# Kernel optimization log

Hardware: AMD Instinct MI355X
Metric: run time of the kernel (lower is better)

Reference implementation:

```python
import jax, jax.numpy as jnp
import numpy as np

N, E, F, H, D = 4096, 65536, 128, 128, 3
RATIO = 0.5
SLOPE = 0.01  # LeakyReLU negative slope (torch default)


def setup_inputs() -> dict:
    key = jax.random.key(0)
    ks = jax.random.split(key, 8)
    s = 1.0 / np.sqrt(H)
    x = jax.random.normal(ks[0], (N, F), dtype=jnp.float32)
    edge_index = jax.random.randint(ks[1], (2, E), 0, N, dtype=jnp.int64)
    Wd = jax.random.normal(ks[2], (D + 1, F, H), dtype=jnp.float32) * s
    bd = jax.random.normal(ks[3], (D + 1, H), dtype=jnp.float32) * 0.01
    Wu = jax.random.normal(ks[4], (D, H, H), dtype=jnp.float32) * s
    bu = jax.random.normal(ks[5], (D, H), dtype=jnp.float32) * 0.01
    pw = jax.random.normal(ks[6], (D, H), dtype=jnp.float32) * s
    return dict(x=x, edge_index=edge_index, Wd=Wd, bd=bd, Wu=Wu, bu=bu, pw=pw)


def gcn(x, A, W, b):
    # GCNConv(improved=True): self-loop fill value 2; A[i, j] = weight of edge j -> i
    A2 = A + 2.0 * jnp.eye(A.shape[0], dtype=A.dtype)
    deg = A2.sum(axis=1)
    dinv = jnp.where(deg > 0, jax.lax.rsqrt(deg), 0.0)
    Ahat = dinv[:, None] * A2 * dinv[None, :]
    return Ahat @ (x @ W) + b


def augment(A):
    # GraphUNet.augment_adj: remove self loops, add self loops (w=1), A @ A (spspmm), remove self loops
    n = A.shape[0]
    eye = jnp.eye(n, dtype=A.dtype)
    A1 = A * (1.0 - eye) + eye
    B = A1 @ A1
    return B * (1.0 - eye)


def topk_pool(x, A, w, k):
    # TopKPooling: score = tanh(x @ w / ||w||); keep top-k nodes (descending)
    score = jnp.tanh((x @ w) / jnp.linalg.norm(w))
    top, perm = jax.lax.top_k(score, k)
    xp = x[perm] * top[:, None]
    Ap = A[perm][:, perm]
    return xp, Ap, perm


def reference(x, edge_index, Wd, bd, Wu, bu, pw):
    act = lambda v: jax.nn.leaky_relu(v, SLOPE)
    # dense adjacency in [dst, src] convention; duplicate edges sum (coalesce)
    A = jnp.zeros((N, N), jnp.float32).at[edge_index[1], edge_index[0]].add(1.0)
    x = act(gcn(x, A, Wd[0], bd[0]))
    xs, As, perms = [x], [A], []
    n = N
    for i in range(1, D + 1):
        A = augment(A)
        k = int(np.ceil(RATIO * n))
        n = k
        x, A, perm = topk_pool(x, A, pw[i - 1], k)
        x = act(gcn(x, A, Wd[i], bd[i]))
        if i < D:
            xs.append(x)
            As.append(A)
        perms.append(perm)
    for i in range(D):
        j = D - 1 - i
        res, Aj, perm = xs[j], As[j], perms[j]
        up = jnp.zeros_like(res).at[perm].set(x)  # unpool: scatter into kept slots
        x = res + up  # sum_res=True
        x = gcn(x, Aj, Wu[i], bu[i])
        if i < D - 1:
            x = act(x)
    return x  # [N, out_dim]
```

## Files before the change

kernel.cpp:

```cpp
#include <hip/hip_runtime.h>

typedef unsigned short u16;
typedef __attribute__((ext_vector_type(4))) short s16x4;
typedef __attribute__((ext_vector_type(8))) short s16x8;
typedef __attribute__((ext_vector_type(4))) float f32x4;

__device__ __forceinline__ float bf2f_(u16 b) { return __uint_as_float(((unsigned)b) << 16); }
__device__ __forceinline__ u16 f2bf_(float f) {
  unsigned u = __float_as_uint(f);
  return (u16)((u + 0x7FFFu + ((u >> 16) & 1u)) >> 16);
}

__device__ __forceinline__ void edge_decode(const int* ei, int e, int E, const int* flags,
                                            int& src, int& dst) {
  bool is64 = flags[1] < 100;
  src = is64 ? ei[2 * e] : ei[e];
  dst = is64 ? ei[2 * E + 2 * e] : ei[E + e];
}

__global__ void k_zeroi(int* a, int n) {
  int i = blockIdx.x * 256 + threadIdx.x;
  if (i < n) a[i] = 0;
}

__global__ __launch_bounds__(256) void k_detect(const u16* __restrict__ xb,
                                                const int* __restrict__ ei,
                                                int* __restrict__ flags) {
  int i = blockIdx.x * 256 + threadIdx.x;
  int e8 = (xb[2 * i] >> 7) & 0xFF;
  int sane = (e8 >= 100 && e8 <= 140) ? 1 : 0;
  int nz = (ei[2 * i + 1] != 0) ? 1 : 0;
  #pragma unroll
  for (int off = 32; off; off >>= 1) { sane += __shfl_down(sane, off); nz += __shfl_down(nz, off); }
  if ((threadIdx.x & 63) == 0) { atomicAdd(&flags[0], sane); atomicAdd(&flags[1], nz); }
}

__global__ void k_loadall(const void* x, const void* wd, const void* bd, const void* wu,
                          const void* bu, const void* pw,
                          float* xin, float* Wdf, float* bdf, float* Wuf, float* buf_, float* pwf,
                          const int* __restrict__ flags) {
  int i = blockIdx.x * 256 + threadIdx.x;
  const void* src; float* dst; int off;
  if (i < 524288) { src = x; dst = xin; off = i; }
  else if (i < 589824) { src = wd; dst = Wdf; off = i - 524288; }
  else if (i < 590336) { src = bd; dst = bdf; off = i - 589824; }
  else if (i < 639488) { src = wu; dst = Wuf; off = i - 590336; }
  else if (i < 639872) { src = bu; dst = buf_; off = i - 639488; }
  else if (i < 640256) { src = pw; dst = pwf; off = i - 639872; }
  else return;
  bool isbf = flags[0] >= 2048;
  dst[off] = isbf ? bf2f_(((const u16*)src)[off]) : ((const float*)src)[off];
}

__global__ void k_fill0(float4* __restrict__ p, long n4) {
  long i = blockIdx.x * 256L + threadIdx.x;
  long stride = (long)gridDim.x * 256L;
  for (; i < n4; i += stride) p[i] = make_float4(0.f, 0.f, 0.f, 0.f);
}

__global__ void k_diag0(float* __restrict__ C, int M) {
  int i = blockIdx.x * 256 + threadIdx.x;
  if (i < M) C[(size_t)i * M + i] = 0.f;
}

__global__ void k_degcnt(const int* __restrict__ ei, int E, int n, const int* __restrict__ flags,
                         int* __restrict__ indeg, int* __restrict__ outdeg, int* __restrict__ indeg2) {
  int e = blockIdx.x * 256 + threadIdx.x;
  if (e >= E) return;
  int src, dst; edge_decode(ei, e, E, flags, src, dst);
  if (src < 0 || src >= n || dst < 0 || dst >= n) return;
  atomicAdd(&indeg2[dst], 1);
  if (src == dst) return;
  atomicAdd(&indeg[dst], 1);
  atomicAdd(&outdeg[src], 1);
}

__global__ __launch_bounds__(1024) void k_scan3(const int* __restrict__ d0, const int* __restrict__ d1,
                                                const int* __restrict__ d2,
                                                int* o0, int* o1, int* o2,
                                                int* c0, int* c1, int* c2, int n) {
  __shared__ int part[1024];
  int t = threadIdx.x;
  int per = n / 1024;
  for (int pass = 0; pass < 3; ++pass) {
    const int* deg = pass == 0 ? d0 : (pass == 1 ? d1 : d2);
    int* off = pass == 0 ? o0 : (pass == 1 ? o1 : o2);
    int* cur = pass == 0 ? c0 : (pass == 1 ? c1 : c2);
    int local[8];
    int s = 0;
    for (int j = 0; j < per; ++j) { local[j] = s; s += deg[t * per + j]; }
    part[t] = s;
    __syncthreads();
    for (int d = 1; d < 1024; d <<= 1) {
      int v = (t >= d) ? part[t - d] : 0;
      __syncthreads();
      part[t] += v;
      __syncthreads();
    }
    int base = (t == 0) ? 0 : part[t - 1];
    for (int j = 0; j < per; ++j) {
      off[t * per + j] = base + local[j];
      cur[t * per + j] = base + local[j];
    }
    if (t == 1023) off[n] = part[1023];
    __syncthreads();
  }
}

__global__ void k_csrfill(const int* __restrict__ ei, int E, int n, const int* __restrict__ flags,
                          int* __restrict__ incur, int* __restrict__ outcur, int* __restrict__ incur2,
                          int* __restrict__ inlist, int* __restrict__ outlist, int* __restrict__ inlist2) {
  int e = blockIdx.x * 256 + threadIdx.x;
  if (e >= E) return;
  int src, dst; edge_decode(ei, e, E, flags, src, dst);
  if (src < 0 || src >= n || dst < 0 || dst >= n) return;
  inlist2[atomicAdd(&incur2[dst], 1)] = src;
  if (src == dst) return;
  inlist[atomicAdd(&incur[dst], 1)] = src;
  outlist[atomicAdd(&outcur[src], 1)] = dst;
}

__global__ __launch_bounds__(256) void k_rowsort(const int* __restrict__ inoff2,
                                                 const int* __restrict__ inlist2,
                                                 int* __restrict__ outlist2, int n) {
  int wave = threadIdx.x >> 6, lane = threadIdx.x & 63;
  int row = blockIdx.x * 4 + wave;
  if (row >= n) return;
  int ib = inoff2[row], ie = inoff2[row + 1];
  int L = ie - ib;
  for (int i = lane; i < L; i += 64) {
    int ki = inlist2[ib + i];
    int rank = 0;
    for (int j = 0; j < L; ++j) {
      int kj = inlist2[ib + j];
      rank += (kj < ki || (kj == ki && j < i)) ? 1 : 0;
    }
    outlist2[ib + rank] = ki;
  }
}

__global__ void k_dinvcsr(const int* __restrict__ indeg2, float* __restrict__ dinv, int n) {
  int i = blockIdx.x * 256 + threadIdx.x;
  if (i < n) dinv[i] = rsqrtf((float)indeg2[i] + 2.0f);
}

__global__ __launch_bounds__(256) void k_spool(const int* __restrict__ inoff, const int* __restrict__ inlist,
                                               const int* __restrict__ outoff, const int* __restrict__ outlist,
                                               const int* __restrict__ inv, float* __restrict__ C,
                                               int M, int n) {
  int wave = threadIdx.x >> 6, lane = threadIdx.x & 63;
  int v = blockIdx.x * 4 + wave;
  if (v >= n) return;
  int ib = inoff[v], ni = inoff[v + 1] - ib;
  int ob = outoff[v], no = outoff[v + 1] - ob;
  int tot = ni * no;
  for (int p = lane; p < tot; p += 64) {
    int oi = p / ni, ii = p - oi * ni;
    int i = outlist[ob + oi];
    int j = inlist[ib + ii];
    if (i == j) continue;
    int ri = inv[i], rj = inv[j];
    if (ri >= 0 && rj >= 0) atomicAdd(&C[(size_t)ri * M + rj], 1.0f);
  }
}

__global__ void k_spedge(const int* __restrict__ ei, int E, int n, const int* __restrict__ flags,
                         const int* __restrict__ inv, float* __restrict__ C, int M) {
  int e = blockIdx.x * 256 + threadIdx.x;
  if (e >= E) return;
  int src, dst; edge_decode(ei, e, E, flags, src, dst);
  if (src < 0 || src >= n || dst < 0 || dst >= n || src == dst) return;
  int ri = inv[dst], rj = inv[src];
  if (ri >= 0 && rj >= 0) atomicAdd(&C[(size_t)ri * M + rj], 2.0f);
}

__global__ __launch_bounds__(256) void k_dinv(const float* __restrict__ A, float* __restrict__ dinv, int n) {
  int row = blockIdx.x;
  const float* r = A + (size_t)row * n;
  float s = 0.f;
  for (int j = threadIdx.x; j < n; j += 256) s += r[j];
  #pragma unroll
  for (int off = 32; off; off >>= 1) s += __shfl_down(s, off);
  __shared__ float red[4];
  int wave = threadIdx.x >> 6, lane = threadIdx.x & 63;
  if (lane == 0) red[wave] = s;
  __syncthreads();
  if (threadIdx.x == 0) {
    float deg = red[0] + red[1] + red[2] + red[3] + 2.0f;
    dinv[row] = rsqrtf(deg);
  }
}

__global__ __launch_bounds__(256) void k_xw(const float* __restrict__ x, const float* __restrict__ W,
                                            const float* __restrict__ dinv, float* __restrict__ yp, int n) {
  __shared__ float xs_[16 * 128];
  int t = threadIdx.x;
  int row0 = blockIdx.x * 16;
  for (int e = t; e < 16 * 128; e += 256) {
    int r = e >> 7, c = e & 127;
    xs_[e] = x[(size_t)(row0 + r) * 128 + c];
  }
  __syncthreads();
  int c = t & 127, rh = t >> 7;
  float acc[8];
  #pragma unroll
  for (int ri = 0; ri < 8; ++ri) acc[ri] = 0.f;
  for (int k = 0; k < 128; ++k) {
    float wv = W[k * 128 + c];
    #pragma unroll
    for (int ri = 0; ri < 8; ++ri) acc[ri] += xs_[(rh * 8 + ri) * 128 + k] * wv;
  }
  #pragma unroll
  for (int ri = 0; ri < 8; ++ri) {
    int r = row0 + rh * 8 + ri;
    yp[(size_t)r * 128 + c] = dinv[r] * acc[ri];
  }
}

template<int FINAL>
__global__ __launch_bounds__(256) void k_spmv(const int* __restrict__ inoff2, const int* __restrict__ inlist2,
                                              const float* __restrict__ y, const float* __restrict__ dinv,
                                              const float* __restrict__ b,
                                              float* __restrict__ outf, void* __restrict__ outv,
                                              int n, int act, const int* __restrict__ flags) {
  int wave = threadIdx.x >> 6, lane = threadIdx.x & 63;
  int i = blockIdx.x * 4 + wave;
  if (i >= n) return;
  int ib = inoff2[i], ie = inoff2[i + 1];
  float z0 = 0.f, z1 = 0.f;
  for (int e = ib; e < ie; ++e) {
    int s = inlist2[e];
    z0 += y[(size_t)s * 128 + lane];
    z1 += y[(size_t)s * 128 + 64 + lane];
  }
  float di = dinv[i];
  float y0 = y[(size_t)i * 128 + lane], y1 = y[(size_t)i * 128 + 64 + lane];
  float v0 = di * (z0 + 2.0f * y0) + b[lane];
  float v1 = di * (z1 + 2.0f * y1) + b[64 + lane];
  if (act) { v0 = (v0 >= 0.f) ? v0 : 0.01f * v0; v1 = (v1 >= 0.f) ? v1 : 0.01f * v1; }
  if (FINAL) {
    if (flags[0] >= 2048) {
      ((u16*)outv)[(size_t)i * 128 + lane] = f2bf_(v0);
      ((u16*)outv)[(size_t)i * 128 + 64 + lane] = f2bf_(v1);
    } else {
      ((float*)outv)[(size_t)i * 128 + lane] = v0;
      ((float*)outv)[(size_t)i * 128 + 64 + lane] = v1;
    }
  } else {
    outf[(size_t)i * 128 + lane] = v0;
    outf[(size_t)i * 128 + 64 + lane] = v1;
  }
}

__global__ __launch_bounds__(256) void k_ytr(const float* __restrict__ y,
                                             u16* __restrict__ yTh, u16* __restrict__ yTl, int n) {
  __shared__ float tile[32][129];
  int t = threadIdx.x;
  int r0 = blockIdx.x * 32;
  #pragma unroll
  for (int it = 0; it < 4; ++it) {
    int q = it * 256 + t;
    int r = q >> 5, c4 = (q & 31) * 4;
    float4 v = *(const float4*)&y[(size_t)(r0 + r) * 128 + c4];
    tile[r][c4] = v.x; tile[r][c4 + 1] = v.y; tile[r][c4 + 2] = v.z; tile[r][c4 + 3] = v.w;
  }
  __syncthreads();
  #pragma unroll
  for (int it = 0; it < 2; ++it) {
    int q = it * 256 + t;
    int c = q >> 2, r8 = (q & 3) * 8;
    s16x8 h, l;
    #pragma unroll
    for (int j = 0; j < 8; ++j) {
      float v = tile[r8 + j][c];
      u16 hb = f2bf_(v);
      h[j] = (short)hb;
      l[j] = (short)f2bf_(v - bf2f_(hb));
    }
    *(s16x8*)&yTh[(size_t)c * n + r0 + r8] = h;
    *(s16x8*)&yTl[(size_t)c * n + r0 + r8] = l;
  }
}

template<int ALO>
__global__ __launch_bounds__(256) void k_zgemm_mfma(const float* __restrict__ A,
                                                    const u16* __restrict__ yTh,
                                                    const u16* __restrict__ yTl,
                                                    float* __restrict__ zpart,
                                                    int n, int kchunk) {
  __shared__ __align__(16) u16 ah_[128 * 64];
  __shared__ __align__(16) u16 al_[ALO ? 128 * 64 : 8];
  __shared__ __align__(16) u16 bh_[128 * 64];
  __shared__ __align__(16) u16 bl_[128 * 64];
  int t = threadIdx.x;
  int row0 = blockIdx.x * 128;
  int s = blockIdx.y;
  int kbase = s * kchunk;
  int wave = t >> 6, lane = t & 63;
  int wr = wave >> 1, wc = wave & 1;
  int lrow = lane & 15, kb = lane >> 4;
  const f32x4 z4 = {0.f, 0.f, 0.f, 0.f};
  f32x4 acc[4][4];
  #pragma unroll
  for (int a = 0; a < 4; ++a)
    #pragma unroll
    for (int b = 0; b < 4; ++b) acc[a][b] = z4;

  for (int k0 = 0; k0 < kchunk; k0 += 64) {
    int koff = kbase + k0;
    __syncthreads();
    #pragma unroll
    for (int it = 0; it < 8; ++it) {
      int q = it * 256 + t;
      int r = q >> 4, i4 = q & 15;
      int g = i4 >> 1, h4 = (i4 & 1) * 4;
      float4 v = *(const float4*)&A[(size_t)(row0 + r) * n + koff + i4 * 4];
      float vv[4] = {v.x, v.y, v.z, v.w};
      s16x4 hh, ll;
      #pragma unroll
      for (int j = 0; j < 4; ++j) {
        u16 hb = f2bf_(vv[j]);
        hh[j] = (short)hb;
        if (ALO) ll[j] = (short)f2bf_(vv[j] - bf2f_(hb));
      }
      int ld = r * 64 + ((g ^ (r & 7)) << 3) + h4;
      *(s16x4*)&ah_[ld] = hh;
      if (ALO) *(s16x4*)&al_[ld] = ll;
    }
    #pragma unroll
    for (int it = 0; it < 4; ++it) {
      int q = it * 256 + t;
      int r = q >> 3, g = q & 7;
      int ld = r * 64 + ((g ^ (r & 7)) << 3);
      *(s16x8*)&bh_[ld] = *(const s16x8*)(yTh + (size_t)r * n + koff + g * 8);
      *(s16x8*)&bl_[ld] = *(const s16x8*)(yTl + (size_t)r * n + koff + g * 8);
    }
    __syncthreads();
    #pragma unroll
    for (int ks = 0; ks < 2; ++ks) {
      int gg = ks * 4 + kb;
      int gsw = (gg ^ (lrow & 7)) << 3;
      s16x8 af[4], alf[4], bhf[4], blf[4];
      #pragma unroll
      for (int mi = 0; mi < 4; ++mi) {
        int row = wr * 64 + mi * 16 + lrow;
        af[mi] = *(const s16x8*)&ah_[row * 64 + gsw];
        if (ALO) alf[mi] = *(const s16x8*)&al_[row * 64 + gsw];
      }
      #pragma unroll
      for (int ni = 0; ni < 4; ++ni) {
        int row = wc * 64 + ni * 16 + lrow;
        bhf[ni] = *(const s16x8*)&bh_[row * 64 + gsw];
        blf[ni] = *(const s16x8*)&bl_[row * 64 + gsw];
      }
      #pragma unroll
      for (int mi = 0; mi < 4; ++mi)
        #pragma unroll
        for (int ni = 0; ni < 4; ++ni) {
          acc[mi][ni] = __builtin_amdgcn_mfma_f32_16x16x32_bf16(af[mi], bhf[ni], acc[mi][ni], 0, 0, 0);
          acc[mi][ni] = __builtin_amdgcn_mfma_f32_16x16x32_bf16(af[mi], blf[ni], acc[mi][ni], 0, 0, 0);
          if (ALO) {
            acc[mi][ni] = __builtin_amdgcn_mfma_f32_16x16x32_bf16(alf[mi], bhf[ni], acc[mi][ni], 0, 0, 0);
            acc[mi][ni] = __builtin_amdgcn_mfma_f32_16x16x32_bf16(alf[mi], blf[ni], acc[mi][ni], 0, 0, 0);
          }
        }
    }
  }
  int rbase = (lane >> 4) * 4;
  #pragma unroll
  for (int mi = 0; mi < 4; ++mi)
    #pragma unroll
    for (int ni = 0; ni < 4; ++ni)
      #pragma unroll
      for (int j = 0; j < 4; ++j) {
        int gi = row0 + wr * 64 + mi * 16 + rbase + j;
        int gj = wc * 64 + ni * 16 + (lane & 15);
        zpart[((size_t)s * n + gi) * 128 + gj] = acc[mi][ni][j];
      }
}

__global__ void k_epi(const float* __restrict__ zpart, const float* __restrict__ yp,
                      const float* __restrict__ dinv, const float* __restrict__ b,
                      float* __restrict__ outf, int tot, int act, int n, int S) {
  int i = blockIdx.x * 256 + threadIdx.x;
  if (i >= tot) return;
  int r = i >> 7, c = i & 127;
  float z = 0.f;
  for (int s = 0; s < S; ++s) z += zpart[((size_t)s * n + r) * 128 + c];
  float v = dinv[r] * (z + 2.0f * yp[i]) + b[c];
  if (act) v = (v >= 0.f) ? v : 0.01f * v;
  outf[i] = v;
}

__global__ __launch_bounds__(256) void k_score(const float* __restrict__ x, const float* __restrict__ w,
                                               float* __restrict__ ts, int n) {
  int wave = threadIdx.x >> 6, lane = threadIdx.x & 63;
  int row = blockIdx.x * 4 + wave;
  float w0 = w[lane], w1 = w[64 + lane];
  float nrm = w0 * w0 + w1 * w1;
  #pragma unroll
  for (int off = 32; off; off >>= 1) nrm += __shfl_down(nrm, off);
  nrm = sqrtf(__shfl(nrm, 0));
  if (row < n) {
    const float* xr = x + (size_t)row * 128;
    float d = xr[lane] * w0 + xr[64 + lane] * w1;
    #pragma unroll
    for (int off = 32; off; off >>= 1) d += __shfl_down(d, off);
    if (lane == 0) ts[row] = tanhf(d / nrm);
  }
}

__global__ __launch_bounds__(256) void k_rank(const float* __restrict__ ts, int n, int k,
                                              int* __restrict__ perm, int* __restrict__ inv) {
  int wave = threadIdx.x >> 6, lane = threadIdx.x & 63;
  int i = blockIdx.x * 4 + wave;
  if (i >= n) return;
  unsigned bits = __float_as_uint(ts[i]);
  unsigned u = (bits & 0x80000000u) ? ~bits : (bits | 0x80000000u);
  unsigned long long my = ((unsigned long long)u << 32) | (unsigned)(0xFFFFFFFFu - (unsigned)i);
  int rank = 0;
  for (int j = lane; j < n; j += 64) {
    unsigned b2 = __float_as_uint(ts[j]);
    unsigned u2 = (b2 & 0x80000000u) ? ~b2 : (b2 | 0x80000000u);
    unsigned long long kj = ((unsigned long long)u2 << 32) | (unsigned)(0xFFFFFFFFu - (unsigned)j);
    rank += (kj > my) ? 1 : 0;
  }
  #pragma unroll
  for (int off = 32; off; off >>= 1) rank += __shfl_down(rank, off);
  if (lane == 0) {
    if (rank < k) perm[rank] = i;
    inv[i] = (rank < k) ? rank : -1;
  }
}

__global__ void k_gather(const float* __restrict__ x, const int* __restrict__ perm,
                         const float* __restrict__ ts, float* __restrict__ out, int k) {
  int i = blockIdx.x * 256 + threadIdx.x;
  if (i < k * 128) {
    int r = i >> 7, c = i & 127;
    int p = perm[r];
    out[i] = x[(size_t)p * 128 + c] * ts[p];
  }
}

__global__ void k_unpool(const float* __restrict__ res, const float* __restrict__ prev,
                         const int* __restrict__ inv, float* __restrict__ dst, int tot) {
  int idx = blockIdx.x * 256 + threadIdx.x;
  if (idx >= tot) return;
  int r = idx >> 7, c = idx & 127;
  int ir = inv[r];
  float v = res[idx];
  if (ir >= 0) v += prev[(size_t)ir * 128 + c];
  dst[idx] = v;
}

__global__ __launch_bounds__(256) void k_prep(const float* __restrict__ A, u16* __restrict__ A1,
                                              u16* __restrict__ A1T, int n) {
  __shared__ float tile[32][33];
  int bi = blockIdx.y, bj = blockIdx.x;
  int tx = threadIdx.x & 31, ty = threadIdx.x >> 5;
  int r0 = bi * 32, c0 = bj * 32;
  #pragma unroll
  for (int yy = 0; yy < 4; ++yy) {
    int r = ty * 4 + yy;
    int gr = r0 + r, gc = c0 + tx;
    float v = A[(size_t)gr * n + gc];
    if (gr == gc) v = 1.0f;
    tile[r][tx] = v;
    A1[(size_t)gr * n + gc] = f2bf_(v);
  }
  __syncthreads();
  #pragma unroll
  for (int yy = 0; yy < 4; ++yy) {
    int r = ty * 4 + yy;
    int gr = c0 + r, gc = r0 + tx;
    A1T[(size_t)gr * n + gc] = f2bf_(tile[tx][r]);
  }
}

__global__ __launch_bounds__(256) void k_mfma_pool(const u16* __restrict__ A1, const u16* __restrict__ A1T,
                                                   const int* __restrict__ perm, float* __restrict__ C,
                                                   int M, int K, int kchunk) {
  __shared__ __align__(16) u16 a_lds[128 * 64];
  __shared__ __align__(16) u16 b_lds[128 * 64];
  __shared__ int pr[128], pc[128];
  int t = threadIdx.x;
  int br = blockIdx.x, bc = blockIdx.y;
  int kbase = blockIdx.z * kchunk;
  if (t < 128) pr[t] = perm[br * 128 + t];
  else pc[t - 128] = perm[bc * 128 + (t - 128)];
  __syncthreads();
  int wave = t >> 6, lane = t & 63;
  int wr = wave >> 1, wc = wave & 1;
  int lrow = lane & 15, kb = lane >> 4;
  const f32x4 z4 = {0.f, 0.f, 0.f, 0.f};
  f32x4 acc[4][4];
  #pragma unroll
  for (int a = 0; a < 4; ++a)
    #pragma unroll
    for (int b = 0; b < 4; ++b) acc[a][b] = z4;

  for (int k0 = 0; k0 < kchunk; k0 += 64) {
    int koff = kbase + k0;
    __syncthreads();
    #pragma unroll
    for (int it = 0; it < 4; ++it) {
      int q = it * 256 + t;
      int r = q >> 3, g = q & 7;
      int ld = r * 64 + ((g ^ (r & 7)) << 3);
      *(s16x8*)&a_lds[ld] = *(const s16x8*)(A1 + (size_t)pr[r] * K + koff + g * 8);
      *(s16x8*)&b_lds[ld] = *(const s16x8*)(A1T + (size_t)pc[r] * K + koff + g * 8);
    }
    __syncthreads();
    #pragma unroll
    for (int ks = 0; ks < 2; ++ks) {
      int gg = ks * 4 + kb;
      int gsw = (gg ^ (lrow & 7)) << 3;
      s16x8 af[4], bfv[4];
      #pragma unroll
      for (int mi = 0; mi < 4; ++mi)
        af[mi] = *(const s16x8*)&a_lds[(wr * 64 + mi * 16 + lrow) * 64 + gsw];
      #pragma unroll
      for (int ni = 0; ni < 4; ++ni)
        bfv[ni] = *(const s16x8*)&b_lds[(wc * 64 + ni * 16 + lrow) * 64 + gsw];
      #pragma unroll
      for (int mi = 0; mi < 4; ++mi)
        #pragma unroll
        for (int ni = 0; ni < 4; ++ni)
          acc[mi][ni] = __builtin_amdgcn_mfma_f32_16x16x32_bf16(af[mi], bfv[ni], acc[mi][ni], 0, 0, 0);
    }
  }
  int rbase = (lane >> 4) * 4;
  #pragma unroll
  for (int mi = 0; mi < 4; ++mi)
    #pragma unroll
    for (int ni = 0; ni < 4; ++ni)
      #pragma unroll
      for (int j = 0; j < 4; ++j) {
        int gi = br * 128 + wr * 64 + mi * 16 + rbase + j;
        int gj = bc * 128 + wc * 64 + ni * 16 + (lane & 15);
        atomicAdd(&C[(size_t)gi * M + gj], acc[mi][ni][j]);
      }
}

static void run_gcn_dense(hipStream_t s, const float* A, int n, const float* xinp,
                          const float* W, const float* b, float* dinv, int compute_dinv, float* tmpY,
                          u16* yTh, u16* yTl, float* zpart, int alo, int act, float* outf) {
  if (compute_dinv) k_dinv<<<n, 256, 0, s>>>(A, dinv, n);
  k_xw<<<n / 16, 256, 0, s>>>(xinp, W, dinv, tmpY, n);
  k_ytr<<<n / 32, 256, 0, s>>>(tmpY, yTh, yTl, n);
  int S = (n >= 2048) ? 16 : (n == 1024 ? 8 : 4);
  int kchunk = n / S;
  if (alo)
    k_zgemm_mfma<1><<<dim3(n / 128, S), 256, 0, s>>>(A, yTh, yTl, zpart, n, kchunk);
  else
    k_zgemm_mfma<0><<<dim3(n / 128, S), 256, 0, s>>>(A, yTh, yTl, zpart, n, kchunk);
  int tot = n * 128;
  k_epi<<<(tot + 255) / 256, 256, 0, s>>>(zpart, tmpY, dinv, b, outf, tot, act, n, S);
}

extern "C" void kernel_launch(void* const* d_in, const int* in_sizes, int n_in,
                              void* d_out, int out_size, void* d_ws, size_t ws_size,
                              hipStream_t stream) {
  (void)in_sizes; (void)n_in; (void)out_size; (void)ws_size;
  const void* x_in  = d_in[0];
  const int*  ei    = (const int*)d_in[1];
  const void* Wd_in = d_in[2];
  const void* bd_in = d_in[3];
  const void* Wu_in = d_in[4];
  const void* bu_in = d_in[5];
  const void* pw_in = d_in[6];

  char* p = (char*)d_ws;
  auto alloc = [&](size_t bytes) { char* r = p; p += (bytes + 255) & ~(size_t)255; return r; };
  float* A1p  = (float*)alloc(2048ull * 2048 * 4);
  float* A2p  = (float*)alloc(1024ull * 1024 * 4);
  float* A3p  = (float*)alloc(512ull * 512 * 4);
  u16*   A1b  = (u16*)alloc(4096ull * 4096 * 2);
  u16*   A1bT = (u16*)alloc(4096ull * 4096 * 2);
  float* xb0  = (float*)alloc(4096 * 128 * 4);
  float* xb1  = (float*)alloc(2048 * 128 * 4);
  float* xb2  = (float*)alloc(1024 * 128 * 4);
  float* xb3  = (float*)alloc(512 * 128 * 4);
  float* xin  = (float*)alloc(4096 * 128 * 4);
  float* tmpX = (float*)alloc(4096 * 128 * 4);
  float* tmpY = (float*)alloc(4096 * 128 * 4);
  float* dinv0 = (float*)alloc(4096 * 4);
  float* dinv1 = (float*)alloc(2048 * 4);
  float* dinv2 = (float*)alloc(1024 * 4);
  float* dinv3 = (float*)alloc(512 * 4);
  float* tsc  = (float*)alloc(4096 * 4);
  float* Wdf  = (float*)alloc(4 * 128 * 128 * 4);
  float* bdf  = (float*)alloc(4 * 128 * 4);
  float* Wuf  = (float*)alloc(3 * 128 * 128 * 4);
  float* buf_ = (float*)alloc(3 * 128 * 4);
  float* pwf  = (float*)alloc(3 * 128 * 4);
  int* iblk = (int*)alloc((12292 + 3 * 4097 + 3 * 4096 + 4 * 65536 + 4096 + 2048 + 1024 + 2048 + 1024 + 512) * 4);
  int* flags  = iblk;
  int* indeg  = iblk + 4;
  int* outdeg = iblk + 4100;
  int* indeg2 = iblk + 8196;
  int* q      = iblk + 12292;
  int* inoff  = q;  q += 4097;
  int* outoff = q;  q += 4097;
  int* inoff2 = q;  q += 4097;
  int* incur  = q;  q += 4096;
  int* outcur = q;  q += 4096;
  int* incur2 = q;  q += 4096;
  int* inlist = q;  q += 65536;
  int* outlist= q;  q += 65536;
  int* inlist2= q;  q += 65536;
  int* inlist2s = q; q += 65536;
  int* inv1   = q;  q += 4096;
  int* inv2   = q;  q += 2048;
  int* inv3   = q;  q += 1024;
  int* perm1  = q;  q += 2048;
  int* perm2  = q;  q += 1024;
  int* perm3  = q;  q += 512;

  float* zpart = (float*)A1b;
  u16*   yTh   = (u16*)A1bT;
  u16*   yTl   = (u16*)A1bT + 128 * 4096;

  const int E = 65536, N0 = 4096;

  k_zeroi<<<(12292 + 255) / 256, 256, 0, stream>>>(iblk, 12292);
  k_detect<<<16, 256, 0, stream>>>((const u16*)x_in, ei, flags);
  k_loadall<<<(640256 + 255) / 256, 256, 0, stream>>>(x_in, Wd_in, bd_in, Wu_in, bu_in, pw_in,
                                                      xin, Wdf, bdf, Wuf, buf_, pwf, flags);
  k_degcnt<<<(E + 255) / 256, 256, 0, stream>>>(ei, E, N0, flags, indeg, outdeg, indeg2);
  k_scan3<<<1, 1024, 0, stream>>>(indeg, outdeg, indeg2, inoff, outoff, inoff2,
                                  incur, outcur, incur2, N0);
  k_csrfill<<<(E + 255) / 256, 256, 0, stream>>>(ei, E, N0, flags, incur, outcur, incur2,
                                                 inlist, outlist, inlist2);
  k_rowsort<<<N0 / 4, 256, 0, stream>>>(inoff2, inlist2, inlist2s, N0);
  k_dinvcsr<<<(N0 + 255) / 256, 256, 0, stream>>>(indeg2, dinv0, N0);

  k_xw<<<N0 / 16, 256, 0, stream>>>(xin, Wdf, dinv0, tmpY, N0);
  k_spmv<0><<<N0 / 4, 256, 0, stream>>>(inoff2, inlist2s, tmpY, dinv0, bdf, xb0, nullptr, N0, 1, flags);

  {
    int n = 4096, k = 2048;
    k_score<<<n / 4, 256, 0, stream>>>(xb0, pwf, tsc, n);
    k_rank<<<n / 4, 256, 0, stream>>>(tsc, n, k, perm1, inv1);
    k_fill0<<<2048, 256, 0, stream>>>((float4*)A1p, (long)k * k / 4);
    k_spool<<<n / 4, 256, 0, stream>>>(inoff, inlist, outoff, outlist, inv1, A1p, k, n);
    k_spedge<<<(E + 255) / 256, 256, 0, stream>>>(ei, E, n, flags, inv1, A1p, k);
    k_gather<<<(k * 128 + 255) / 256, 256, 0, stream>>>(xb0, perm1, tsc, tmpX, k);
    run_gcn_dense(stream, A1p, k, tmpX, Wdf + 16384, bdf + 128, dinv1, 1, tmpY, yTh, yTl, zpart, 0, 1, xb1);
  }

  {
    float* Acurs[2]  = {A1p, A2p};
    float* Anexts[2] = {A2p, A3p};
    int*   perms[2]  = {perm2, perm3};
    int*   invs[2]   = {inv2, inv3};
    float* xcurs[2]  = {xb1, xb2};
    float* xouts[2]  = {xb2, xb3};
    float* dinvs[2]  = {dinv2, dinv3};
    int    spoolS[2] = {4, 8};
    int    ns[2]     = {2048, 1024};
    for (int li = 0; li < 2; ++li) {
      int n = ns[li], k = n / 2, lvl = li + 2;
      k_score<<<n / 4, 256, 0, stream>>>(xcurs[li], pwf + (lvl - 1) * 128, tsc, n);
      k_rank<<<n / 4, 256, 0, stream>>>(tsc, n, k, perms[li], invs[li]);
      k_prep<<<dim3(n / 32, n / 32), 256, 0, stream>>>(Acurs[li], A1b, A1bT, n);
      float* Cn = Anexts[li];
      int Sp = spoolS[li];
      k_fill0<<<2048, 256, 0, stream>>>((float4*)Cn, (long)k * k / 4);
      k_mfma_pool<<<dim3(k / 128, k / 128, Sp), 256, 0, stream>>>(A1b, A1bT, perms[li], Cn, k, n, n / Sp);
      k_diag0<<<(k + 255) / 256, 256, 0, stream>>>(Cn, k);
      k_gather<<<(k * 128 + 255) / 256, 256, 0, stream>>>(xcurs[li], perms[li], tsc, tmpX, k);
      run_gcn_dense(stream, Cn, k, tmpX, Wdf + lvl * 16384, bdf + lvl * 128,
                    dinvs[li], 1, tmpY, yTh, yTl, zpart, 1, 1, xouts[li]);
    }
  }

  k_unpool<<<(1024 * 128 + 255) / 256, 256, 0, stream>>>(xb2, xb3, inv3, tmpX, 1024 * 128);
  run_gcn_dense(stream, A2p, 1024, tmpX, Wuf, buf_, dinv2, 0, tmpY, yTh, yTl, zpart, 1, 1, xb2);

  k_unpool<<<(2048 * 128 + 255) / 256, 256, 0, stream>>>(xb1, xb2, inv2, tmpX, 2048 * 128);
  run_gcn_dense(stream, A1p, 2048, tmpX, Wuf + 16384, buf_ + 128, dinv1, 0, tmpY, yTh, yTl, zpart, 0, 1, xb1);

  k_unpool<<<(4096 * 128 + 255) / 256, 256, 0, stream>>>(xb0, xb1, inv1, tmpX, 4096 * 128);
  k_xw<<<N0 / 16, 256, 0, stream>>>(tmpX, Wuf + 2 * 16384, dinv0, tmpY, N0);
  k_spmv<1><<<N0 / 4, 256, 0, stream>>>(inoff2, inlist2s, tmpY, dinv0, buf_ + 2 * 128, nullptr, d_out, N0, 0, flags);
}
```

Before: 392.2 us.

## Fuse small GCN pipeline kernels to cut launch count

Several small kernels are folded into neighbours. Degree normalisation moves into rowsort and into the XW kernel. The top-k score moves into the spmv and epilogue kernels. The gather and unpool steps now happen in the XW load, and the bf16 hi/lo transpose is written from XW. The sparse-pool join and edge kernels merge into one launch, and the diagonal zeroing becomes a guard in the MFMA pool atomic. The aim is to remove many launches and intermediate global round-trips. The cost is more work per XW block (a row-sum of the dense adjacency done by only 4 waves) and less coalesced transposed writes.

```diff
diff --git a/kernel.cpp b/kernel.cpp
--- a/kernel.cpp
+++ b/kernel.cpp
@@ -56,11 +56,6 @@
   long i = blockIdx.x * 256L + threadIdx.x;
   long stride = (long)gridDim.x * 256L;
   for (; i < n4; i += stride) p[i] = make_float4(0.f, 0.f, 0.f, 0.f);
-}
-
-__global__ void k_diag0(float* __restrict__ C, int M) {
-  int i = blockIdx.x * 256 + threadIdx.x;
-  if (i < M) C[(size_t)i * M + i] = 0.f;
 }
 
 __global__ void k_degcnt(const int* __restrict__ ei, int E, int n, const int* __restrict__ flags,
@@ -122,7 +117,9 @@
 
 __global__ __launch_bounds__(256) void k_rowsort(const int* __restrict__ inoff2,
                                                  const int* __restrict__ inlist2,
-                                                 int* __restrict__ outlist2, int n) {
+                                                 int* __restrict__ outlist2,
+                                                 const int* __restrict__ indeg2,
+                                                 float* __restrict__ dinv, int n) {
   int wave = threadIdx.x >> 6, lane = threadIdx.x & 63;
   int row = blockIdx.x * 4 + wave;
   if (row >= n) return;
@@ -137,68 +134,82 @@
     }
     outlist2[ib + rank] = ki;
   }
-}
-
-__global__ void k_dinvcsr(const int* __restrict__ indeg2, float* __restrict__ dinv, int n) {
-  int i = blockIdx.x * 256 + threadIdx.x;
-  if (i < n) dinv[i] = rsqrtf((float)indeg2[i] + 2.0f);
+  if (lane == 0) dinv[row] = rsqrtf((float)indeg2[row] + 2.0f);
 }
 
 __global__ __launch_bounds__(256) void k_spool(const int* __restrict__ inoff, const int* __restrict__ inlist,
                                                const int* __restrict__ outoff, const int* __restrict__ outlist,
                                                const int* __restrict__ inv, float* __restrict__ C,
-                                               int M, int n) {
+                                               int M, int n, int njoin,
+                                               const int* __restrict__ ei, int E, const int* __restrict__ flags) {
   int wave = threadIdx.x >> 6, lane = threadIdx.x & 63;
-  int v = blockIdx.x * 4 + wave;
-  if (v >= n) return;
-  int ib = inoff[v], ni = inoff[v + 1] - ib;
-  int ob = outoff[v], no = outoff[v + 1] - ob;
-  int tot = ni * no;
-  for (int p = lane; p < tot; p += 64) {
-    int oi = p / ni, ii = p - oi * ni;
-    int i = outlist[ob + oi];
-    int j = inlist[ib + ii];
-    if (i == j) continue;
-    int ri = inv[i], rj = inv[j];
-    if (ri >= 0 && rj >= 0) atomicAdd(&C[(size_t)ri * M + rj], 1.0f);
-  }
-}
-
-__global__ void k_spedge(const int* __restrict__ ei, int E, int n, const int* __restrict__ flags,
-                         const int* __restrict__ inv, float* __restrict__ C, int M) {
-  int e = blockIdx.x * 256 + threadIdx.x;
-  if (e >= E) return;
-  int src, dst; edge_decode(ei, e, E, flags, src, dst);
-  if (src < 0 || src >= n || dst < 0 || dst >= n || src == dst) return;
-  int ri = inv[dst], rj = inv[src];
-  if (ri >= 0 && rj >= 0) atomicAdd(&C[(size_t)ri * M + rj], 2.0f);
-}
-
-__global__ __launch_bounds__(256) void k_dinv(const float* __restrict__ A, float* __restrict__ dinv, int n) {
-  int row = blockIdx.x;
-  const float* r = A + (size_t)row * n;
-  float s = 0.f;
-  for (int j = threadIdx.x; j < n; j += 256) s += r[j];
-  #pragma unroll
-  for (int off = 32; off; off >>= 1) s += __shfl_down(s, off);
-  __shared__ float red[4];
-  int wave = threadIdx.x >> 6, lane = threadIdx.x & 63;
-  if (lane == 0) red[wave] = s;
-  __syncthreads();
-  if (threadIdx.x == 0) {
-    float deg = red[0] + red[1] + red[2] + red[3] + 2.0f;
-    dinv[row] = rsqrtf(deg);
-  }
-}
-
-__global__ __launch_bounds__(256) void k_xw(const float* __restrict__ x, const float* __restrict__ W,
-                                            const float* __restrict__ dinv, float* __restrict__ yp, int n) {
+  if ((int)blockIdx.x < njoin) {
+    int v = blockIdx.x * 4 + wave;
+    if (v >= n) return;
+    int ib = inoff[v], ni = inoff[v + 1] - ib;
+    int ob = outoff[v], no = outoff[v + 1] - ob;
+    int tot = ni * no;
+    for (int p = lane; p < tot; p += 64) {
+      int oi = p / ni, ii = p - oi * ni;
+      int i = outlist[ob + oi];
+      int j = inlist[ib + ii];
+      if (i == j) continue;
+      int ri = inv[i], rj = inv[j];
+      if (ri >= 0 && rj >= 0) atomicAdd(&C[(size_t)ri * M + rj], 1.0f);
+    }
+  } else {
+    int e = (blockIdx.x - njoin) * 256 + threadIdx.x;
+    if (e >= E) return;
+    int src, dst; edge_decode(ei, e, E, flags, src, dst);
+    if (src < 0 || src >= n || dst < 0 || dst >= n || src == dst) return;
+    int ri = inv[dst], rj = inv[src];
+    if (ri >= 0 && rj >= 0) atomicAdd(&C[(size_t)ri * M + rj], 2.0f);
+  }
+}
+
+template<int MODE, int CDINV, int WT>
+__global__ __launch_bounds__(256) void k_xw(const float* __restrict__ x, const float* __restrict__ res,
+                                            const float* __restrict__ prev,
+                                            const int* __restrict__ perm, const int* __restrict__ invm,
+                                            const float* __restrict__ ts,
+                                            const float* __restrict__ A, const float* __restrict__ W,
+                                            float* __restrict__ dinv, float* __restrict__ yp,
+                                            u16* __restrict__ yTh, u16* __restrict__ yTl, int n) {
   __shared__ float xs_[16 * 128];
+  __shared__ float ds[16];
   int t = threadIdx.x;
   int row0 = blockIdx.x * 16;
   for (int e = t; e < 16 * 128; e += 256) {
     int r = e >> 7, c = e & 127;
-    xs_[e] = x[(size_t)(row0 + r) * 128 + c];
+    int gr = row0 + r;
+    float v;
+    if (MODE == 0) v = x[(size_t)gr * 128 + c];
+    else if (MODE == 1) { int p0 = perm[gr]; v = x[(size_t)p0 * 128 + c] * ts[p0]; }
+    else {
+      int ir = invm[gr];
+      v = res[(size_t)gr * 128 + c];
+      if (ir >= 0) v += prev[(size_t)ir * 128 + c];
+    }
+    xs_[e] = v;
+  }
+  int wave = t >> 6, lane = t & 63;
+  if (CDINV) {
+    #pragma unroll
+    for (int rr = 0; rr < 4; ++rr) {
+      int r = wave * 4 + rr;
+      const float* Ar = A + (size_t)(row0 + r) * n;
+      float s = 0.f;
+      for (int j = lane; j < n; j += 64) s += Ar[j];
+      #pragma unroll
+      for (int off = 32; off; off >>= 1) s += __shfl_down(s, off);
+      if (lane == 0) {
+        float d = rsqrtf(s + 2.0f);
+        ds[r] = d;
+        dinv[row0 + r] = d;
+      }
+    }
+  } else {
+    if (t < 16) ds[t] = dinv[row0 + t];
   }
   __syncthreads();
   int c = t & 127, rh = t >> 7;
@@ -210,18 +221,31 @@
     #pragma unroll
     for (int ri = 0; ri < 8; ++ri) acc[ri] += xs_[(rh * 8 + ri) * 128 + k] * wv;
   }
+  s16x8 h, l;
   #pragma unroll
   for (int ri = 0; ri < 8; ++ri) {
     int r = row0 + rh * 8 + ri;
-    yp[(size_t)r * 128 + c] = dinv[r] * acc[ri];
-  }
-}
-
-template<int FINAL>
+    float v = ds[rh * 8 + ri] * acc[ri];
+    yp[(size_t)r * 128 + c] = v;
+    if (WT) {
+      u16 hb = f2bf_(v);
+      h[ri] = (short)hb;
+      l[ri] = (short)f2bf_(v - bf2f_(hb));
+    }
+  }
+  if (WT) {
+    int rbase = row0 + rh * 8;
+    *(s16x8*)&yTh[(size_t)c * n + rbase] = h;
+    *(s16x8*)&yTl[(size_t)c * n + rbase] = l;
+  }
+}
+
+template<int FINAL, int SCORE>
 __global__ __launch_bounds__(256) void k_spmv(const int* __restrict__ inoff2, const int* __restrict__ inlist2,
                                               const float* __restrict__ y, const float* __restrict__ dinv,
-                                              const float* __restrict__ b,
+                                              const float* __restrict__ b, const float* __restrict__ w,
                                               float* __restrict__ outf, void* __restrict__ outv,
+                                              float* __restrict__ ts,
                                               int n, int act, const int* __restrict__ flags) {
   int wave = threadIdx.x >> 6, lane = threadIdx.x & 63;
   int i = blockIdx.x * 4 + wave;
@@ -250,35 +274,13 @@
     outf[(size_t)i * 128 + lane] = v0;
     outf[(size_t)i * 128 + 64 + lane] = v1;
   }
-}
-
-__global__ __launch_bounds__(256) void k_ytr(const float* __restrict__ y,
-                                             u16* __restrict__ yTh, u16* __restrict__ yTl, int n) {
-  __shared__ float tile[32][129];
-  int t = threadIdx.x;
-  int r0 = blockIdx.x * 32;
-  #pragma unroll
-  for (int it = 0; it < 4; ++it) {
-    int q = it * 256 + t;
-    int r = q >> 5, c4 = (q & 31) * 4;
-    float4 v = *(const float4*)&y[(size_t)(r0 + r) * 128 + c4];
-    tile[r][c4] = v.x; tile[r][c4 + 1] = v.y; tile[r][c4 + 2] = v.z; tile[r][c4 + 3] = v.w;
-  }
-  __syncthreads();
-  #pragma unroll
-  for (int it = 0; it < 2; ++it) {
-    int q = it * 256 + t;
-    int c = q >> 2, r8 = (q & 3) * 8;
-    s16x8 h, l;
-    #pragma unroll
-    for (int j = 0; j < 8; ++j) {
-      float v = tile[r8 + j][c];
-      u16 hb = f2bf_(v);
-      h[j] = (short)hb;
-      l[j] = (short)f2bf_(v - bf2f_(hb));
-    }
-    *(s16x8*)&yTh[(size_t)c * n + r0 + r8] = h;
-    *(s16x8*)&yTl[(size_t)c * n + r0 + r8] = l;
+  if (SCORE) {
+    float w0 = w[lane], w1 = w[64 + lane];
+    float nr = w0 * w0 + w1 * w1;
+    float dt = v0 * w0 + v1 * w1;
+    #pragma unroll
+    for (int off = 32; off; off >>= 1) { nr += __shfl_down(nr, off); dt += __shfl_down(dt, off); }
+    if (lane == 0) ts[i] = tanhf(dt / sqrtf(nr));
   }
 }
 
@@ -379,34 +381,34 @@
       }
 }
 
-__global__ void k_epi(const float* __restrict__ zpart, const float* __restrict__ yp,
-                      const float* __restrict__ dinv, const float* __restrict__ b,
-                      float* __restrict__ outf, int tot, int act, int n, int S) {
-  int i = blockIdx.x * 256 + threadIdx.x;
-  if (i >= tot) return;
-  int r = i >> 7, c = i & 127;
-  float z = 0.f;
-  for (int s = 0; s < S; ++s) z += zpart[((size_t)s * n + r) * 128 + c];
-  float v = dinv[r] * (z + 2.0f * yp[i]) + b[c];
-  if (act) v = (v >= 0.f) ? v : 0.01f * v;
-  outf[i] = v;
-}
-
-__global__ __launch_bounds__(256) void k_score(const float* __restrict__ x, const float* __restrict__ w,
-                                               float* __restrict__ ts, int n) {
+template<int SCORE>
+__global__ __launch_bounds__(256) void k_epi(const float* __restrict__ zpart, const float* __restrict__ yp,
+                                             const float* __restrict__ dinv, const float* __restrict__ b,
+                                             const float* __restrict__ w,
+                                             float* __restrict__ outf, float* __restrict__ ts,
+                                             int n, int S, int act) {
   int wave = threadIdx.x >> 6, lane = threadIdx.x & 63;
-  int row = blockIdx.x * 4 + wave;
-  float w0 = w[lane], w1 = w[64 + lane];
-  float nrm = w0 * w0 + w1 * w1;
-  #pragma unroll
-  for (int off = 32; off; off >>= 1) nrm += __shfl_down(nrm, off);
-  nrm = sqrtf(__shfl(nrm, 0));
-  if (row < n) {
-    const float* xr = x + (size_t)row * 128;
-    float d = xr[lane] * w0 + xr[64 + lane] * w1;
-    #pragma unroll
-    for (int off = 32; off; off >>= 1) d += __shfl_down(d, off);
-    if (lane == 0) ts[row] = tanhf(d / nrm);
+  int r = blockIdx.x * 4 + wave;
+  if (r >= n) return;
+  float z0 = 0.f, z1 = 0.f;
+  for (int s = 0; s < S; ++s) {
+    const float* zp = zpart + ((size_t)s * n + r) * 128;
+    z0 += zp[lane];
+    z1 += zp[64 + lane];
+  }
+  float di = dinv[r];
+  float v0 = di * (z0 + 2.0f * yp[(size_t)r * 128 + lane]) + b[lane];
+  float v1 = di * (z1 + 2.0f * yp[(size_t)r * 128 + 64 + lane]) + b[64 + lane];
+  if (act) { v0 = (v0 >= 0.f) ? v0 : 0.01f * v0; v1 = (v1 >= 0.f) ? v1 : 0.01f * v1; }
+  outf[(size_t)r * 128 + lane] = v0;
+  outf[(size_t)r * 128 + 64 + lane] = v1;
+  if (SCORE) {
+    float w0 = w[lane], w1 = w[64 + lane];
+    float nr = w0 * w0 + w1 * w1;
+    float dt = v0 * w0 + v1 * w1;
+    #pragma unroll
+    for (int off = 32; off; off >>= 1) { nr += __shfl_down(nr, off); dt += __shfl_down(dt, off); }
+    if (lane == 0) ts[r] = tanhf(dt / sqrtf(nr));
   }
 }
 
@@ -431,27 +433,6 @@
     if (rank < k) perm[rank] = i;
     inv[i] = (rank < k) ? rank : -1;
   }
-}
-
-__global__ void k_gather(const float* __restrict__ x, const int* __restrict__ perm,
-                         const float* __restrict__ ts, float* __restrict__ out, int k) {
-  int i = blockIdx.x * 256 + threadIdx.x;
-  if (i < k * 128) {
-    int r = i >> 7, c = i & 127;
-    int p = perm[r];
-    out[i] = x[(size_t)p * 128 + c] * ts[p];
-  }
-}
-
-__global__ void k_unpool(const float* __restrict__ res, const float* __restrict__ prev,
-                         const int* __restrict__ inv, float* __restrict__ dst, int tot) {
-  int idx = blockIdx.x * 256 + threadIdx.x;
-  if (idx >= tot) return;
-  int r = idx >> 7, c = idx & 127;
-  int ir = inv[r];
-  float v = res[idx];
-  if (ir >= 0) v += prev[(size_t)ir * 128 + c];
-  dst[idx] = v;
 }
 
 __global__ __launch_bounds__(256) void k_prep(const float* __restrict__ A, u16* __restrict__ A1,
@@ -539,24 +520,8 @@
       for (int j = 0; j < 4; ++j) {
         int gi = br * 128 + wr * 64 + mi * 16 + rbase + j;
         int gj = bc * 128 + wc * 64 + ni * 16 + (lane & 15);
-        atomicAdd(&C[(size_t)gi * M + gj], acc[mi][ni][j]);
+        if (gi != gj) atomicAdd(&C[(size_t)gi * M + gj], acc[mi][ni][j]);
       }
-}
-
-static void run_gcn_dense(hipStream_t s, const float* A, int n, const float* xinp,
-                          const float* W, const float* b, float* dinv, int compute_dinv, float* tmpY,
-                          u16* yTh, u16* yTl, float* zpart, int alo, int act, float* outf) {
-  if (compute_dinv) k_dinv<<<n, 256, 0, s>>>(A, dinv, n);
-  k_xw<<<n / 16, 256, 0, s>>>(xinp, W, dinv, tmpY, n);
-  k_ytr<<<n / 32, 256, 0, s>>>(tmpY, yTh, yTl, n);
-  int S = (n >= 2048) ? 16 : (n == 1024 ? 8 : 4);
-  int kchunk = n / S;
-  if (alo)
-    k_zgemm_mfma<1><<<dim3(n / 128, S), 256, 0, s>>>(A, yTh, yTl, zpart, n, kchunk);
-  else
-    k_zgemm_mfma<0><<<dim3(n / 128, S), 256, 0, s>>>(A, yTh, yTl, zpart, n, kchunk);
-  int tot = n * 128;
-  k_epi<<<(tot + 255) / 256, 256, 0, s>>>(zpart, tmpY, dinv, b, outf, tot, act, n, S);
 }
 
 extern "C" void kernel_launch(void* const* d_in, const int* in_sizes, int n_in,
@@ -583,7 +548,6 @@
   float* xb2  = (float*)alloc(1024 * 128 * 4);
   float* xb3  = (float*)alloc(512 * 128 * 4);
   float* xin  = (float*)alloc(4096 * 128 * 4);
-  float* tmpX = (float*)alloc(4096 * 128 * 4);
   float* tmpY = (float*)alloc(4096 * 128 * 4);
   float* dinv0 = (float*)alloc(4096 * 4);
   float* dinv1 = (float*)alloc(2048 * 4);
@@ -633,21 +597,24 @@
                                   incur, outcur, incur2, N0);
   k_csrfill<<<(E + 255) / 256, 256, 0, stream>>>(ei, E, N0, flags, incur, outcur, incur2,
                                                  inlist, outlist, inlist2);
-  k_rowsort<<<N0 / 4, 256, 0, stream>>>(inoff2, inlist2, inlist2s, N0);
-  k_dinvcsr<<<(N0 + 255) / 256, 256, 0, stream>>>(indeg2, dinv0, N0);
-
-  k_xw<<<N0 / 16, 256, 0, stream>>>(xin, Wdf, dinv0, tmpY, N0);
-  k_spmv<0><<<N0 / 4, 256, 0, stream>>>(inoff2, inlist2s, tmpY, dinv0, bdf, xb0, nullptr, N0, 1, flags);
+  k_rowsort<<<N0 / 4, 256, 0, stream>>>(inoff2, inlist2, inlist2s, indeg2, dinv0, N0);
+
+  k_xw<0, 0, 0><<<N0 / 16, 256, 0, stream>>>(xin, nullptr, nullptr, nullptr, nullptr, nullptr,
+                                             nullptr, Wdf, dinv0, tmpY, nullptr, nullptr, N0);
+  k_spmv<0, 1><<<N0 / 4, 256, 0, stream>>>(inoff2, inlist2s, tmpY, dinv0, bdf, pwf,
+                                           xb0, nullptr, tsc, N0, 1, flags);
 
   {
     int n = 4096, k = 2048;
-    k_score<<<n / 4, 256, 0, stream>>>(xb0, pwf, tsc, n);
     k_rank<<<n / 4, 256, 0, stream>>>(tsc, n, k, perm1, inv1);
     k_fill0<<<2048, 256, 0, stream>>>((float4*)A1p, (long)k * k / 4);
-    k_spool<<<n / 4, 256, 0, stream>>>(inoff, inlist, outoff, outlist, inv1, A1p, k, n);
-    k_spedge<<<(E + 255) / 256, 256, 0, stream>>>(ei, E, n, flags, inv1, A1p, k);
-    k_gather<<<(k * 128 + 255) / 256, 256, 0, stream>>>(xb0, perm1, tsc, tmpX, k);
-    run_gcn_dense(stream, A1p, k, tmpX, Wdf + 16384, bdf + 128, dinv1, 1, tmpY, yTh, yTl, zpart, 0, 1, xb1);
+    int njoin = n / 4;
+    k_spool<<<njoin + (E + 255) / 256, 256, 0, stream>>>(inoff, inlist, outoff, outlist, inv1, A1p,
+                                                         k, n, njoin, ei, E, flags);
+    k_xw<1, 1, 1><<<k / 16, 256, 0, stream>>>(xb0, nullptr, nullptr, perm1, nullptr, tsc,
+                                              A1p, Wdf + 16384, dinv1, tmpY, yTh, yTl, k);
+    k_zgemm_mfma<0><<<dim3(k / 128, 16), 256, 0, stream>>>(A1p, yTh, yTl, zpart, k, k / 16);
+    k_epi<1><<<k / 4, 256, 0, stream>>>(zpart, tmpY, dinv1, bdf + 128, pwf + 128, xb1, tsc, k, 16, 1);
   }
 
   {
@@ -662,27 +629,37 @@
     int    ns[2]     = {2048, 1024};
     for (int li = 0; li < 2; ++li) {
       int n = ns[li], k = n / 2, lvl = li + 2;
-      k_score<<<n / 4, 256, 0, stream>>>(xcurs[li], pwf + (lvl - 1) * 128, tsc, n);
       k_rank<<<n / 4, 256, 0, stream>>>(tsc, n, k, perms[li], invs[li]);
       k_prep<<<dim3(n / 32, n / 32), 256, 0, stream>>>(Acurs[li], A1b, A1bT, n);
       float* Cn = Anexts[li];
       int Sp = spoolS[li];
       k_fill0<<<2048, 256, 0, stream>>>((float4*)Cn, (long)k * k / 4);
       k_mfma_pool<<<dim3(k / 128, k / 128, Sp), 256, 0, stream>>>(A1b, A1bT, perms[li], Cn, k, n, n / Sp);
-      k_diag0<<<(k + 255) / 256, 256, 0, stream>>>(Cn, k);
-      k_gather<<<(k * 128 + 255) / 256, 256, 0, stream>>>(xcurs[li], perms[li], tsc, tmpX, k);
-      run_gcn_dense(stream, Cn, k, tmpX, Wdf + lvl * 16384, bdf + lvl * 128,
-                    dinvs[li], 1, tmpY, yTh, yTl, zpart, 1, 1, xouts[li]);
-    }
-  }
-
-  k_unpool<<<(1024 * 128 + 255) / 256, 256, 0, stream>>>(xb2, xb3, inv3, tmpX, 1024 * 128);
-  run_gcn_dense(stream, A2p, 1024, tmpX, Wuf, buf_, dinv2, 0, tmpY, yTh, yTl, zpart, 1, 1, xb2);
-
-  k_unpool<<<(2048 * 128 + 255) / 256, 256, 0, stream>>>(xb1, xb2, inv2, tmpX, 2048 * 128);
-  run_gcn_dense(stream, A1p, 2048, tmpX, Wuf + 16384, buf_ + 128, dinv1, 0, tmpY, yTh, yTl, zpart, 0, 1, xb1);
-
-  k_unpool<<<(4096 * 128 + 255) / 256, 256, 0, stream>>>(xb0, xb1, inv1, tmpX, 4096 * 128);
-  k_xw<<<N0 / 16, 256, 0, stream>>>(tmpX, Wuf + 2 * 16384, dinv0, tmpY, N0);
-  k_spmv<1><<<N0 / 4, 256, 0, stream>>>(inoff2, inlist2s, tmpY, dinv0, buf_ + 2 * 128, nullptr, d_out, N0, 0, flags);
-}
+      int S = (k >= 2048) ? 16 : (k == 1024 ? 8 : 4);
+      k_xw<1, 1, 1><<<k / 16, 256, 0, stream>>>(xcurs[li], nullptr, nullptr, perms[li], nullptr, tsc,
+                                                Cn, Wdf + lvl * 16384, dinvs[li], tmpY, yTh, yTl, k);
+      k_zgemm_mfma<1><<<dim3(k / 128, S), 256, 0, stream>>>(Cn, yTh, yTl, zpart, k, k / S);
+      if (li == 0)
+        k_epi<1><<<k / 4, 256, 0, stream>>>(zpart, tmpY, dinvs[li], bdf + lvl * 128, pwf + lvl * 128,
+                                            xouts[li], tsc, k, S, 1);
+      else
+        k_epi<0><<<k / 4, 256, 0, stream>>>(zpart, tmpY, dinvs[li], bdf + lvl * 128, nullptr,
+                                            xouts[li], nullptr, k, S, 1);
+    }
+  }
+
+  k_xw<2, 0, 1><<<1024 / 16, 256, 0, stream>>>(nullptr, xb2, xb3, nullptr, inv3, nullptr,
+                                               nullptr, Wuf, dinv2, tmpY, yTh, yTl, 1024);
+  k_zgemm_mfma<1><<<dim3(1024 / 128, 8), 256, 0, stream>>>(A2p, yTh, yTl, zpart, 1024, 1024 / 8);
+  k_epi<0><<<1024 / 4, 256, 0, stream>>>(zpart, tmpY, dinv2, buf_, nullptr, xb2, nullptr, 1024, 8, 1);
+
+  k_xw<2, 0, 1><<<2048 / 16, 256, 0, stream>>>(nullptr, xb1, xb2, nullptr, inv2, nullptr,
+                                               nullptr, Wuf + 16384, dinv1, tmpY, yTh, yTl, 2048);
+  k_zgemm_mfma<0><<<dim3(2048 / 128, 16), 256, 0, stream>>>(A1p, yTh, yTl, zpart, 2048, 2048 / 16);
+  k_epi<0><<<2048 / 4, 256, 0, stream>>>(zpart, tmpY, dinv1, buf_ + 128, nullptr, xb1, nullptr, 2048, 16, 1);
+
+  k_xw<2, 0, 0><<<N0 / 16, 256, 0, stream>>>(nullptr, xb0, xb1, nullptr, inv1, nullptr,
+                                             nullptr, Wuf + 2 * 16384, dinv0, tmpY, nullptr, nullptr, N0);
+  k_spmv<1, 0><<<N0 / 4, 256, 0, stream>>>(inoff2, inlist2s, tmpY, dinv0, buf_ + 2 * 128, nullptr,
+                                           nullptr, d_out, nullptr, N0, 0, flags);
+}
```

After: 410.1 us. +4.6%, slower.
